# Optimization experiments

Hardware: AMD Instinct MI355X
Metric: run time of the kernel (lower is better)

The kernel has to match this reference:

```python
import jax, jax.numpy as jnp
import numpy as np

WINDOW = 7
SHIFT = 3
NUM_HEADS = 12
DIM = 384
FFN = 4 * DIM
EPS = 1e-5


def _rel_pos_index(w):
    coords = np.stack(np.meshgrid(np.arange(w), np.arange(w), indexing='ij'))  # [2,w,w]
    flat = coords.reshape(2, -1)
    rel = (flat[:, :, None] - flat[:, None, :]).transpose(1, 2, 0)  # [w*w, w*w, 2]
    rel[..., 0] += w - 1
    rel[..., 1] += w - 1
    rel[..., 0] *= 2 * w - 1
    return rel.sum(-1).astype(np.int32)  # [w*w, w*w]


def _attn_mask(hp, wp, w, s):
    # replicate get_attn_mask: region labeling, window partition, pairwise diff
    img = np.zeros((hp, wp), dtype=np.float32)
    cnt = 0
    for hs in (slice(0, -w), slice(-w, -s), slice(-s, None)):
        for ws in (slice(0, -w), slice(-w, -s), slice(-s, None)):
            img[hs, ws] = cnt
            cnt += 1
    mw = img.reshape(hp // w, w, wp // w, w).transpose(0, 2, 1, 3).reshape(-1, w * w)
    diff = mw[:, None, :] - mw[:, :, None]  # unsqueeze(1) - unsqueeze(2)
    return jnp.asarray(np.where(diff != 0, -100.0, 0.0).astype(np.float32))


def _ln(x, g, b):
    mu = jnp.mean(x, -1, keepdims=True)
    var = jnp.mean(jnp.square(x - mu), -1, keepdims=True)
    return (x - mu) * jax.lax.rsqrt(var + EPS) * g + b


def setup_inputs() -> dict:
    key = jax.random.key(0)
    ks = jax.random.split(key, 12)
    B, H, W, C = 8, 56, 56, DIM
    sd = 0.02
    inp = {
        'hidden_states': jax.random.normal(ks[0], (B, H * W, C), jnp.float32),
        'ln1_g': jnp.ones((C,), jnp.float32), 'ln1_b': jnp.zeros((C,), jnp.float32),
        'q_w': jax.random.normal(ks[1], (C, C), jnp.float32) * sd, 'q_b': jnp.zeros((C,), jnp.float32),
        'k_w': jax.random.normal(ks[2], (C, C), jnp.float32) * sd, 'k_b': jnp.zeros((C,), jnp.float32),
        'v_w': jax.random.normal(ks[3], (C, C), jnp.float32) * sd, 'v_b': jnp.zeros((C,), jnp.float32),
        'rpb_table': jax.random.normal(ks[4], ((2 * WINDOW - 1) ** 2, NUM_HEADS), jnp.float32) * sd,
        'rp_index': jnp.asarray(_rel_pos_index(WINDOW)),
        'proj_w': jax.random.normal(ks[5], (C, C), jnp.float32) * sd, 'proj_b': jnp.zeros((C,), jnp.float32),
        'ln2_g': jnp.ones((C,), jnp.float32), 'ln2_b': jnp.zeros((C,), jnp.float32),
        'fc1_w': jax.random.normal(ks[6], (C, FFN), jnp.float32) * sd, 'fc1_b': jnp.zeros((FFN,), jnp.float32),
        'fc2_w': jax.random.normal(ks[7], (FFN, C), jnp.float32) * sd, 'fc2_b': jnp.zeros((C,), jnp.float32),
        'height': H, 'width': W,
    }
    return inp


def reference(hidden_states, ln1_g, ln1_b, q_w, q_b, k_w, k_b, v_w, v_b,
              rpb_table, rp_index, proj_w, proj_b, ln2_g, ln2_b,
              fc1_w, fc1_b, fc2_w, fc2_b, height, width):
    w, s, nh = WINDOW, SHIFT, NUM_HEADS
    B, L, C = hidden_states.shape
    hd = C // nh
    shortcut = hidden_states

    x = _ln(hidden_states, ln1_g, ln1_b).reshape(B, height, width, C)
    pad_b = (w - height % w) % w
    pad_r = (w - width % w) % w
    if pad_b or pad_r:
        x = jnp.pad(x, ((0, 0), (0, pad_b), (0, pad_r), (0, 0)))
    Hp, Wp = height + pad_b, width + pad_r

    if s > 0:
        x = jnp.roll(x, shift=(-s, -s), axis=(1, 2))

    # window partition -> [B*nW, w*w, C]
    N = w * w
    xw = x.reshape(B, Hp // w, w, Wp // w, w, C).transpose(0, 1, 3, 2, 4, 5).reshape(-1, N, C)

    q = (xw @ q_w + q_b).reshape(-1, N, nh, hd).transpose(0, 2, 1, 3)
    k = (xw @ k_w + k_b).reshape(-1, N, nh, hd).transpose(0, 2, 1, 3)
    v = (xw @ v_w + v_b).reshape(-1, N, nh, hd).transpose(0, 2, 1, 3)

    scores = jnp.einsum('whnd,whmd->whnm', q, k) / jnp.sqrt(jnp.float32(hd))
    bias = rpb_table[rp_index.reshape(-1)].reshape(N, N, nh).transpose(2, 0, 1)
    scores = scores + bias[None]

    if s > 0:
        mask = _attn_mask(Hp, Wp, w, s)  # [nW, N, N]
        nW = mask.shape[0]
        scores = scores.reshape(B, nW, nh, N, N) + mask[None, :, None]
        scores = scores.reshape(-1, nh, N, N)

    probs = jax.nn.softmax(scores, axis=-1)
    ctx = jnp.einsum('whnm,whmd->whnd', probs, v).transpose(0, 2, 1, 3).reshape(-1, N, C)
    attn_out = ctx @ proj_w + proj_b

    # window reverse
    xr = attn_out.reshape(B, Hp // w, Wp // w, w, w, C).transpose(0, 1, 3, 2, 4, 5).reshape(B, Hp, Wp, C)
    if s > 0:
        xr = jnp.roll(xr, shift=(s, s), axis=(1, 2))
    if pad_b or pad_r:
        xr = xr[:, :height, :width, :]
    xr = xr.reshape(B, height * width, C)

    h = shortcut + xr
    y = _ln(h, ln2_g, ln2_b)
    y = jax.nn.gelu(y @ fc1_w + fc1_b, approximate=False)
    return h + (y @ fc2_w + fc2_b)
```

## Files before the change

### kernel.cpp

```cpp
#include <hip/hip_runtime.h>
#include <hip/hip_bf16.h>

typedef unsigned short u16;
typedef short bf16x8 __attribute__((ext_vector_type(8)));
typedef float f32x4 __attribute__((ext_vector_type(4)));

__device__ __forceinline__ u16 f2bf(float x) {
  __hip_bfloat16 h = __float2bfloat16(x);
  return *reinterpret_cast<u16*>(&h);
}
__device__ __forceinline__ float bf2f(u16 x) {
  __hip_bfloat16 h = *reinterpret_cast<__hip_bfloat16*>(&x);
  return __bfloat162float(h);
}
__device__ __forceinline__ float rdany(const void* p, size_t i, int f) {
  return f ? ((const float*)p)[i] : bf2f(((const u16*)p)[i]);
}

__device__ __forceinline__ void gld_lds16(const u16* g, u16* l) {
  __builtin_amdgcn_global_load_lds(
      (const __attribute__((address_space(1))) void*)g,
      (__attribute__((address_space(3))) void*)l, 16, 0, 0);
}

__device__ __forceinline__ float gelu_fast(float x) {
  float x2 = x * x;
  float u2 = 1.5957691216057308f * x * __builtin_fmaf(0.044715f, x2, 1.f);
  float e = __expf(u2);
  float r = 1.f / (e + 1.f);
  return x - x * r;
}

__global__ void detect_k(const u16* __restrict__ ln1g_raw, int* __restrict__ flag) {
  if (threadIdx.x == 0 && blockIdx.x == 0)
    *flag = (ln1g_raw[0] == 0 && ln1g_raw[2] == 0) ? 1 : 0;
}

__global__ __launch_bounds__(256) void prep_k(
    const void* qw, const void* kw, const void* vw, const void* pw,
    const void* f1w, const void* f2w,
    u16* __restrict__ qwT, u16* __restrict__ kwT, u16* __restrict__ vwT,
    u16* __restrict__ pwT, u16* __restrict__ f1T, u16* __restrict__ f2T,
    const void* s0, const void* s1, const void* s2, const void* s3,
    const void* s4, const void* s5, const void* s6, const void* s7,
    const void* s8, const void* s9, const void* s10,
    u16* __restrict__ vecdst, const int* __restrict__ rpi,
    u16* __restrict__ biasT, const int* __restrict__ flag) {
  int f = *flag;
  int b = blockIdx.x;
  if (b >= 1728) {
    int tid = threadIdx.y * 32 + threadIdx.x;
    if (b == 1729) {
      for (int i = tid; i < 28812; i += 256) {
        int hh = i / 2401, r = i - hh * 2401;
        biasT[i] = f2bf(rdany(s10, (size_t)rpi[r] * 12 + hh, f));
      }
      return;
    }
    const void* srcs[11] = {s0, s1, s2, s3, s4, s5, s6, s7, s8, s9, s10};
    const int offs[12] = {0, 384, 768, 1152, 1536, 1920, 2304, 2688, 3072, 3456, 4992, 7020};
    for (int i = tid; i < 7020; i += 256) {
      int seg = 0;
#pragma unroll
      for (int t = 1; t < 11; t++) seg += (i >= offs[t]) ? 1 : 0;
      vecdst[i] = f2bf(rdany(srcs[seg], i - offs[seg], f));
    }
    return;
  }
  const void* src; u16* dst; int R, C, bx, by;
  if (b < 576) {
    int m = b / 144, t = b - m * 144;
    src = (m == 0) ? qw : (m == 1) ? kw : (m == 2) ? vw : pw;
    dst = (m == 0) ? qwT : (m == 1) ? kwT : (m == 2) ? vwT : pwT;
    R = 384; C = 384; bx = t % 12; by = t / 12;
  } else if (b < 1152) {
    int t = b - 576; src = f1w; dst = f1T; R = 384; C = 1536;
    bx = t % 48; by = t / 48;
  } else {
    int t = b - 1152; src = f2w; dst = f2T; R = 1536; C = 384;
    bx = t % 12; by = t / 12;
  }
  __shared__ u16 tbuf[32][33];
  int x = threadIdx.x, y = threadIdx.y;
  int gx = bx * 32, gy = by * 32;
#pragma unroll
  for (int j = 0; j < 32; j += 8)
    tbuf[y + j][x] = f2bf(rdany(src, (size_t)(gy + y + j) * C + gx + x, f));
  __syncthreads();
#pragma unroll
  for (int j = 0; j < 32; j += 8) dst[(size_t)(gx + y + j) * R + gy + x] = tbuf[x][y + j];
}

__global__ __launch_bounds__(256) void ln1_window_k(
    const void* __restrict__ hid, const u16* __restrict__ g,
    const u16* __restrict__ b, u16* __restrict__ xw, int rowoff,
    const int* __restrict__ flag) {
  int f = *flag;
  int wv = threadIdx.x >> 6, lane = threadIdx.x & 63;
  int lrow = blockIdx.x * 4 + wv;
  int row = rowoff + lrow;
  int wid = row / 49, n = row - wid * 49;
  int bimg = wid >> 6, w8 = wid & 63;
  int wi = w8 >> 3, wj = w8 & 7;
  int p = n / 7, q = n - p * 7;
  int si = wi * 7 + p + 3; if (si >= 56) si -= 56;
  int sj = wj * 7 + q + 3; if (sj >= 56) sj -= 56;
  size_t src = ((size_t)bimg * 3136 + si * 56 + sj) * 384;
  float x[6]; float s = 0.f, s2 = 0.f;
#pragma unroll
  for (int e = 0; e < 6; e++) {
    x[e] = rdany(hid, src + e * 64 + lane, f);
    s += x[e]; s2 += x[e] * x[e];
  }
#pragma unroll
  for (int off = 32; off; off >>= 1) { s += __shfl_xor(s, off); s2 += __shfl_xor(s2, off); }
  float mu = s * (1.f / 384.f);
  float var = s2 * (1.f / 384.f) - mu * mu;
  float rs = 1.f / sqrtf(var + 1e-5f);
  size_t dst = (size_t)lrow * 384;
#pragma unroll
  for (int e = 0; e < 6; e++) {
    int c = e * 64 + lane;
    float yv = (x[e] - mu) * rs * bf2f(g[c]) + bf2f(b[c]);
    xw[dst + c] = f2bf(yv);
  }
}

__global__ __launch_bounds__(256) void ln2_k(
    const float* hsrc, const u16* __restrict__ g,
    const u16* __restrict__ b, u16* __restrict__ out) {
  int wv = threadIdx.x >> 6, lane = threadIdx.x & 63;
  int row = blockIdx.x * 4 + wv;
  size_t src = (size_t)row * 384;
  float x[6]; float s = 0.f, s2 = 0.f;
#pragma unroll
  for (int e = 0; e < 6; e++) {
    x[e] = hsrc[src + e * 64 + lane];
    s += x[e]; s2 += x[e] * x[e];
  }
#pragma unroll
  for (int off = 32; off; off >>= 1) { s += __shfl_xor(s, off); s2 += __shfl_xor(s2, off); }
  float mu = s * (1.f / 384.f);
  float var = s2 * (1.f / 384.f) - mu * mu;
  float rs = 1.f / sqrtf(var + 1e-5f);
#pragma unroll
  for (int e = 0; e < 6; e++) {
    int c = e * 64 + lane;
    float yv = (x[e] - mu) * rs * bf2f(g[c]) + bf2f(b[c]);
    out[src + c] = f2bf(yv);
  }
}

template <int EPI>
__global__ __launch_bounds__(256, 4) void gemm_bt(
    const u16* __restrict__ A, const u16* __restrict__ Bt,
    const u16* __restrict__ bias, void* outB,
    const void* __restrict__ shortcut, const float* hres,
    int M, int N, int K, int gmoff, int gx, const int* __restrict__ flag) {
  __shared__ __align__(16) u16 As[2][128 * 32];
  __shared__ __align__(16) u16 Bs[2][128 * 32];
  int bx = blockIdx.x;
  if (bx >= gx) return;
  int tid = threadIdx.x;
  int m0 = bx * 128, n0 = blockIdx.y * 128;
  int lane = tid & 63, wv = tid >> 6;
  int wm = (wv >> 1) * 64, wn = (wv & 1) * 64;
  int l15 = lane & 15, quad = lane >> 4;
  f32x4 acc[4][4];
#pragma unroll
  for (int a = 0; a < 4; a++)
#pragma unroll
    for (int c = 0; c < 4; c++) acc[a][c] = (f32x4){0.f, 0.f, 0.f, 0.f};

  int rowS[2], cS[2], wbS[2];
#pragma unroll
  for (int i = 0; i < 2; i++) {
    int id = i * 256 + tid;
    rowS[i] = id >> 2;
    cS[i] = id & 3;
    wbS[i] = (id & ~63) * 8;
  }
  const u16* pA[2]; const u16* pB[2];
#pragma unroll
  for (int i = 0; i < 2; i++) {
    pA[i] = A + (size_t)(m0 + rowS[i]) * K + cS[i] * 8;
    pB[i] = Bt + (size_t)(n0 + rowS[i]) * K + cS[i] * 8;
  }

#pragma unroll
  for (int i = 0; i < 2; i++) {
    gld_lds16(pA[i], &As[0][wbS[i]]);
    gld_lds16(pB[i], &Bs[0][wbS[i]]);
  }
#pragma unroll
  for (int i = 0; i < 2; i++) { pA[i] += 32; pB[i] += 32; }

  int cur = 0;
  for (int kb = 0; kb < K; kb += 32) {
    if (kb + 32 < K) {
#pragma unroll
      for (int i = 0; i < 2; i++) {
        gld_lds16(pA[i], &As[cur ^ 1][wbS[i]]);
        gld_lds16(pB[i], &Bs[cur ^ 1][wbS[i]]);
      }
#pragma unroll
      for (int i = 0; i < 2; i++) { pA[i] += 32; pB[i] += 32; }
      asm volatile("s_waitcnt vmcnt(4)" ::: "memory");
    } else {
      asm volatile("s_waitcnt vmcnt(0)" ::: "memory");
    }
    __builtin_amdgcn_s_barrier();
    __builtin_amdgcn_sched_barrier(0);
    __builtin_amdgcn_s_setprio(1);
    {
      bf16x8 af[4], bfv[4];
#pragma unroll
      for (int mi = 0; mi < 4; mi++)
        af[mi] = *(const bf16x8*)&As[cur][(wm + mi * 16 + l15) * 32 + quad * 8];
#pragma unroll
      for (int ni = 0; ni < 4; ni++)
        bfv[ni] = *(const bf16x8*)&Bs[cur][(wn + ni * 16 + l15) * 32 + quad * 8];
#pragma unroll
      for (int mi = 0; mi < 4; mi++)
#pragma unroll
        for (int ni = 0; ni < 4; ni++)
          acc[mi][ni] = __builtin_amdgcn_mfma_f32_16x16x32_bf16(af[mi], bfv[ni], acc[mi][ni], 0, 0, 0);
    }
    __builtin_amdgcn_s_setprio(0);
    __builtin_amdgcn_sched_barrier(0);
    __builtin_amdgcn_s_barrier();
    cur ^= 1;
  }

  int f = (EPI == 2) ? *flag : 0;
  float biasv[4];
#pragma unroll
  for (int ni = 0; ni < 4; ni++) biasv[ni] = bf2f(bias[n0 + wn + ni * 16 + l15]);
  int seg = n0 / 384;
#pragma unroll
  for (int mi = 0; mi < 4; mi++) {
#pragma unroll
    for (int r = 0; r < 4; r++) {
      int gm = m0 + wm + mi * 16 + quad * 4 + r;
      size_t orow = 0;
      if (EPI == 2) {
        int grow = gmoff + gm;
        int wid = grow / 49, nIn = grow - wid * 49;
        int bimg = wid >> 6, w8 = wid & 63;
        int wi = w8 >> 3, wj = w8 & 7;
        int p = nIn / 7, q = nIn - p * 7;
        int oi = wi * 7 + p + 3; if (oi >= 56) oi -= 56;
        int oj = wj * 7 + q + 3; if (oj >= 56) oj -= 56;
        orow = ((size_t)bimg * 3136 + oi * 56 + oj) * 384;
      }
#pragma unroll
      for (int ni = 0; ni < 4; ni++) {
        int gn = n0 + wn + ni * 16 + l15;
        float v = acc[mi][ni][r] + biasv[ni];
        if (EPI == 1) {
          v = gelu_fast(v);
          ((u16*)outB)[(size_t)gm * N + gn] = f2bf(v);
        } else if (EPI == 2) {
          float hv = rdany(shortcut, orow + gn, f) + v;
          hv = fminf(fmaxf(hv, -1000.f), 1000.f);
          ((float*)outB)[orow + gn] = hv;
        } else if (EPI == 3) {
          float t = v + hres[(size_t)gm * N + gn];
          t = fminf(fmaxf(t, -1000.f), 1000.f);
          ((float*)outB)[(size_t)gm * N + gn] = t;
        } else {
          u16* dst = (u16*)outB + (size_t)seg * M * 384;
          dst[(size_t)gm * 384 + (gn - seg * 384)] = f2bf(v);
        }
      }
    }
  }
}

__global__ __launch_bounds__(256, 5) void attn_k(
    const u16* __restrict__ Q, const u16* __restrict__ Kb, const u16* __restrict__ V,
    const u16* __restrict__ biasT, u16* __restrict__ ctx, int wdoff) {
  __shared__ __align__(16) u16 qs[64 * 56];
  __shared__ __align__(16) u16 ks_[64 * 56];
  __shared__ __align__(16) u16 vt[32 * 72];
  __shared__ __align__(16) u16 P[64 * 72];
  __shared__ int regid[49];
  int lwd = blockIdx.x, hh = blockIdx.y;
  int wd = wdoff + lwd;
  int tid = threadIdx.x;
  int w8 = wd & 63, wi = w8 >> 3, wj = w8 & 7;

  for (int idx = tid; idx < 840; idx += 256) {
    int rr = idx / 56, cc = idx - rr * 56;
    qs[(49 + rr) * 56 + cc] = 0;
    ks_[(49 + rr) * 56 + cc] = 0;
  }
  for (int idx = tid; idx < 480; idx += 256) {
    int d = idx / 15, m = 49 + (idx - d * 15);
    vt[d * 72 + m] = 0;
  }
  if (tid < 49) {
    int p = tid / 7, q = tid - p * 7;
    int rr = (wi == 7) ? (p < 4 ? 1 : 2) : 0;
    int cc = (wj == 7) ? (q < 4 ? 1 : 2) : 0;
    regid[tid] = rr * 3 + cc;
  }
  size_t base = ((size_t)lwd * 49) * 384 + hh * 32;
  for (int idx = tid; idx < 392; idx += 256) {
    int mat = idx >= 196;
    int rid = idx - mat * 196;
    int n = rid >> 2, c = rid & 3;
    uint4 val = *(const uint4*)((mat ? Kb : Q) + base + (size_t)n * 384 + c * 8);
    *(uint4*)&((mat ? ks_ : qs)[n * 56 + c * 8]) = val;
  }
  for (int idx = tid; idx < 196; idx += 256) {
    int n = idx >> 2, c = idx & 3;
    uint4 val = *(const uint4*)(V + base + (size_t)n * 384 + c * 8);
    u16 tmp[8];
    *(uint4*)tmp = val;
#pragma unroll
    for (int t = 0; t < 8; t++) vt[(c * 8 + t) * 72 + n] = tmp[t];
  }
  __syncthreads();

  int lane = tid & 63, wv = tid >> 6, l15 = lane & 15, quad = lane >> 4;
  f32x4 zero = (f32x4){0.f, 0.f, 0.f, 0.f};
  bf16x8 aq = *(const bf16x8*)&qs[(wv * 16 + l15) * 56 + quad * 8];
  f32x4 sc[4];
#pragma unroll
  for (int mi = 0; mi < 4; mi++) {
    bf16x8 bk = *(const bf16x8*)&ks_[(mi * 16 + l15) * 56 + quad * 8];
    sc[mi] = __builtin_amdgcn_mfma_f32_16x16x32_bf16(aq, bk, zero, 0, 0, 0);
  }
  const float scale = 0.17677669529663687f;

  int rm[4];
#pragma unroll
  for (int mi = 0; mi < 4; mi++) {
    int m = mi * 16 + l15;
    rm[mi] = (m < 49) ? regid[m] : -2;
  }
  float pv[4][4];
#pragma unroll
  for (int r = 0; r < 4; r++) {
    int n = wv * 16 + quad * 4 + r;
    int rn = (n < 49) ? regid[n] : -1;
    const u16* brow = biasT + hh * 2401 + n * 49;
#pragma unroll
    for (int mi = 0; mi < 4; mi++) {
      int m = mi * 16 + l15;
      float v = sc[mi][r] * scale;
      if (n < 49 && m < 49) {
        v += bf2f(brow[m]);
        if (rn != rm[mi]) v -= 100.f;
      }
      if (m >= 49) v = -1e4f;
      pv[r][mi] = v;
    }
    float mx = fmaxf(fmaxf(pv[r][0], pv[r][1]), fmaxf(pv[r][2], pv[r][3]));
#pragma unroll
    for (int off = 1; off < 16; off <<= 1) mx = fmaxf(mx, __shfl_xor(mx, off));
    float sum = 0.f;
#pragma unroll
    for (int mi = 0; mi < 4; mi++) {
      pv[r][mi] = __expf(pv[r][mi] - mx);
      sum += pv[r][mi];
    }
#pragma unroll
    for (int off = 1; off < 16; off <<= 1) sum += __shfl_xor(sum, off);
    float inv = 1.f / sum;
#pragma unroll
    for (int mi = 0; mi < 4; mi++)
      P[n * 72 + mi * 16 + l15] = f2bf(pv[r][mi] * inv);
  }

  f32x4 oacc[2]; oacc[0] = zero; oacc[1] = zero;
#pragma unroll
  for (int ks = 0; ks < 2; ks++) {
    bf16x8 ap = *(const bf16x8*)&P[(wv * 16 + l15) * 72 + ks * 32 + quad * 8];
#pragma unroll
    for (int ni = 0; ni < 2; ni++) {
      bf16x8 bv = *(const bf16x8*)&vt[(ni * 16 + l15) * 72 + ks * 32 + quad * 8];
      oacc[ni] = __builtin_amdgcn_mfma_f32_16x16x32_bf16(ap, bv, oacc[ni], 0, 0, 0);
    }
  }
#pragma unroll
  for (int ni = 0; ni < 2; ni++) {
#pragma unroll
    for (int r = 0; r < 4; r++) {
      int n = wv * 16 + quad * 4 + r;
      if (n < 49) {
        int d = ni * 16 + l15;
        ctx[base + (size_t)n * 384 + d] = f2bf(oacc[ni][r]);
      }
    }
  }
}

static inline int pad8(int gx) { return (gx + 7) & ~7; }

extern "C" void kernel_launch(void* const* d_in, const int* in_sizes, int n_in,
                              void* d_out, int out_size, void* d_ws, size_t ws_size,
                              hipStream_t stream) {
  const void* hid = d_in[0];
  const void* ln1g = d_in[1];
  const void* ln1b = d_in[2];
  const void* qw = d_in[3];
  const void* qb = d_in[4];
  const void* kw = d_in[5];
  const void* kbias = d_in[6];
  const void* vw = d_in[7];
  const void* vb = d_in[8];
  const void* rpb = d_in[9];
  const int* rpi = (const int*)d_in[10];
  const void* pw = d_in[11];
  const void* pb = d_in[12];
  const void* ln2g = d_in[13];
  const void* ln2b = d_in[14];
  const void* f1w = d_in[15];
  const void* f1b = d_in[16];
  const void* f2w = d_in[17];
  const void* f2b = d_in[18];

  char* ws = (char*)d_ws;
  u16* wT = (u16*)ws;
  u16* qwT = wT;
  u16* kwT = qwT + 147456;
  u16* vwT = kwT + 147456;
  u16* pwT = vwT + 147456;
  u16* f1T = pwT + 147456;
  u16* f2T = f1T + 589824;
  u16* VEC = (u16*)(ws + 3538944);
  u16* s_ln1g = VEC + 0;
  u16* s_ln1b = VEC + 384;
  u16* s_qkvb = VEC + 768;
  u16* s_pb = VEC + 1920;
  u16* s_ln2g = VEC + 2304;
  u16* s_ln2b = VEC + 2688;
  u16* s_f2b = VEC + 3072;
  u16* s_f1b = VEC + 3456;
  u16* s_rpb = VEC + 4992;
  int* flag = (int*)(ws + 3552984);
  u16* biasT = (u16*)(ws + 3552992);
  const size_t head = 3610624;

  size_t avail = (ws_size > head) ? ws_size - head : 0;
  int rows1 = (avail >= (size_t)25088 * 3072) ? 25088
            : (avail >= (size_t)12544 * 3072) ? 12544 : 6272;
  int rows2 = (avail >= (size_t)25088 * 3840) ? 25088
            : (avail >= (size_t)12544 * 3840) ? 12544 : 3584;

  u16* P1 = (u16*)(ws + head);
  u16* xw = P1;
  u16* Qb = P1 + (size_t)rows1 * 384;
  u16* Kb = Qb + (size_t)rows1 * 384;
  u16* Vb = Kb + (size_t)rows1 * 384;
  u16* y2 = P1;
  u16* f1o = P1 + (size_t)rows2 * 384;
  float* hbuf = (float*)d_out;

  detect_k<<<1, 64, 0, stream>>>((const u16*)ln1g, flag);
  dim3 tb(32, 8);
  prep_k<<<1730, tb, 0, stream>>>(qw, kw, vw, pw, f1w, f2w,
                                  qwT, kwT, vwT, pwT, f1T, f2T,
                                  ln1g, ln1b, qb, kbias, vb, pb, ln2g, ln2b,
                                  f2b, f1b, rpb, VEC, rpi, biasT, flag);

  for (int off = 0; off < 25088; off += rows1) {
    int gx = rows1 / 128;
    ln1_window_k<<<rows1 / 4, 256, 0, stream>>>(hid, s_ln1g, s_ln1b, xw, off, flag);
    gemm_bt<4><<<dim3(pad8(gx), 9), 256, 0, stream>>>(
        xw, qwT, s_qkvb, Qb, nullptr, nullptr, rows1, 1152, 384, 0, gx, flag);
    attn_k<<<dim3(rows1 / 49, 12), 256, 0, stream>>>(Qb, Kb, Vb, biasT, xw, off / 49);
    gemm_bt<2><<<dim3(pad8(gx), 3), 256, 0, stream>>>(
        xw, pwT, s_pb, hbuf, hid, nullptr, rows1, 384, 384, off, gx, flag);
  }

  for (int off = 0; off < 25088; off += rows2) {
    int gx = rows2 / 128;
    ln2_k<<<rows2 / 4, 256, 0, stream>>>(hbuf + (size_t)off * 384, s_ln2g, s_ln2b, y2);
    gemm_bt<1><<<dim3(pad8(gx), 12), 256, 0, stream>>>(
        y2, f1T, s_f1b, f1o, nullptr, nullptr, rows2, 1536, 384, 0, gx, flag);
    gemm_bt<3><<<dim3(pad8(gx), 3), 256, 0, stream>>>(
        f1o, f2T, s_f2b, hbuf + (size_t)off * 384, nullptr,
        hbuf + (size_t)off * 384, rows2, 384, 1536, 0, gx, flag);
  }
}
```

Measured before the change: 397.1 us.

## Replace direct global-to-LDS loads with register-staged loads into padded LDS tiles

The GEMM mainloop no longer uses global_load_lds to write tiles straight into shared memory. Each thread now loads 16 bytes into registers, computes on the current buffer, then writes the prefetched data into a padded LDS layout (row stride 36 instead of 32) to reduce bank conflicts on fragment reads. Fragment reads are split into two 8-byte LDS loads because the padding breaks 16-byte alignment. The change trades away the async direct-to-LDS path, adding register pressure, extra LDS instructions and an additional barrier per K step.

```diff
diff --git a/kernel.cpp b/kernel.cpp
--- a/kernel.cpp
+++ b/kernel.cpp
@@ -15,12 +15,6 @@
 }
 __device__ __forceinline__ float rdany(const void* p, size_t i, int f) {
   return f ? ((const float*)p)[i] : bf2f(((const u16*)p)[i]);
-}
-
-__device__ __forceinline__ void gld_lds16(const u16* g, u16* l) {
-  __builtin_amdgcn_global_load_lds(
-      (const __attribute__((address_space(1))) void*)g,
-      (__attribute__((address_space(3))) void*)l, 16, 0, 0);
 }
 
 __device__ __forceinline__ float gelu_fast(float x) {
@@ -157,8 +151,8 @@
     const u16* __restrict__ bias, void* outB,
     const void* __restrict__ shortcut, const float* hres,
     int M, int N, int K, int gmoff, int gx, const int* __restrict__ flag) {
-  __shared__ __align__(16) u16 As[2][128 * 32];
-  __shared__ __align__(16) u16 Bs[2][128 * 32];
+  __shared__ __align__(16) u16 As[2][128 * 36];
+  __shared__ __align__(16) u16 Bs[2][128 * 36];
   int bx = blockIdx.x;
   if (bx >= gx) return;
   int tid = threadIdx.x;
@@ -172,13 +166,13 @@
 #pragma unroll
     for (int c = 0; c < 4; c++) acc[a][c] = (f32x4){0.f, 0.f, 0.f, 0.f};
 
-  int rowS[2], cS[2], wbS[2];
+  int rowS[2], cS[2], ldsW[2];
 #pragma unroll
   for (int i = 0; i < 2; i++) {
     int id = i * 256 + tid;
     rowS[i] = id >> 2;
     cS[i] = id & 3;
-    wbS[i] = (id & ~63) * 8;
+    ldsW[i] = rowS[i] * 36 + cS[i] * 8;
   }
   const u16* pA[2]; const u16* pB[2];
 #pragma unroll
@@ -187,39 +181,49 @@
     pB[i] = Bt + (size_t)(n0 + rowS[i]) * K + cS[i] * 8;
   }
 
+  uint4 ra[2], rb[2];
+#pragma unroll
+  for (int i = 0; i < 2; i++) { ra[i] = *(const uint4*)pA[i]; rb[i] = *(const uint4*)pB[i]; }
+#pragma unroll
+  for (int i = 0; i < 2; i++) { pA[i] += 32; pB[i] += 32; }
 #pragma unroll
   for (int i = 0; i < 2; i++) {
-    gld_lds16(pA[i], &As[0][wbS[i]]);
-    gld_lds16(pB[i], &Bs[0][wbS[i]]);
-  }
-#pragma unroll
-  for (int i = 0; i < 2; i++) { pA[i] += 32; pB[i] += 32; }
+    *(uint2*)&As[0][ldsW[i]] = make_uint2(ra[i].x, ra[i].y);
+    *(uint2*)&As[0][ldsW[i] + 4] = make_uint2(ra[i].z, ra[i].w);
+    *(uint2*)&Bs[0][ldsW[i]] = make_uint2(rb[i].x, rb[i].y);
+    *(uint2*)&Bs[0][ldsW[i] + 4] = make_uint2(rb[i].z, rb[i].w);
+  }
+  __syncthreads();
 
   int cur = 0;
   for (int kb = 0; kb < K; kb += 32) {
-    if (kb + 32 < K) {
-#pragma unroll
-      for (int i = 0; i < 2; i++) {
-        gld_lds16(pA[i], &As[cur ^ 1][wbS[i]]);
-        gld_lds16(pB[i], &Bs[cur ^ 1][wbS[i]]);
-      }
+    bool more = (kb + 32 < K);
+    if (more) {
+#pragma unroll
+      for (int i = 0; i < 2; i++) { ra[i] = *(const uint4*)pA[i]; rb[i] = *(const uint4*)pB[i]; }
 #pragma unroll
       for (int i = 0; i < 2; i++) { pA[i] += 32; pB[i] += 32; }
-      asm volatile("s_waitcnt vmcnt(4)" ::: "memory");
-    } else {
-      asm volatile("s_waitcnt vmcnt(0)" ::: "memory");
-    }
-    __builtin_amdgcn_s_barrier();
+    }
     __builtin_amdgcn_sched_barrier(0);
     __builtin_amdgcn_s_setprio(1);
     {
       bf16x8 af[4], bfv[4];
 #pragma unroll
-      for (int mi = 0; mi < 4; mi++)
-        af[mi] = *(const bf16x8*)&As[cur][(wm + mi * 16 + l15) * 32 + quad * 8];
-#pragma unroll
-      for (int ni = 0; ni < 4; ni++)
-        bfv[ni] = *(const bf16x8*)&Bs[cur][(wn + ni * 16 + l15) * 32 + quad * 8];
+      for (int mi = 0; mi < 4; mi++) {
+        int base = (wm + mi * 16 + l15) * 36 + quad * 8;
+        union { uint2 h[2]; bf16x8 v; } u;
+        u.h[0] = *(const uint2*)&As[cur][base];
+        u.h[1] = *(const uint2*)&As[cur][base + 4];
+        af[mi] = u.v;
+      }
+#pragma unroll
+      for (int ni = 0; ni < 4; ni++) {
+        int base = (wn + ni * 16 + l15) * 36 + quad * 8;
+        union { uint2 h[2]; bf16x8 v; } u;
+        u.h[0] = *(const uint2*)&Bs[cur][base];
+        u.h[1] = *(const uint2*)&Bs[cur][base + 4];
+        bfv[ni] = u.v;
+      }
 #pragma unroll
       for (int mi = 0; mi < 4; mi++)
 #pragma unroll
@@ -228,7 +232,17 @@
     }
     __builtin_amdgcn_s_setprio(0);
     __builtin_amdgcn_sched_barrier(0);
-    __builtin_amdgcn_s_barrier();
+    __syncthreads();
+    if (more) {
+#pragma unroll
+      for (int i = 0; i < 2; i++) {
+        *(uint2*)&As[cur ^ 1][ldsW[i]] = make_uint2(ra[i].x, ra[i].y);
+        *(uint2*)&As[cur ^ 1][ldsW[i] + 4] = make_uint2(ra[i].z, ra[i].w);
+        *(uint2*)&Bs[cur ^ 1][ldsW[i]] = make_uint2(rb[i].x, rb[i].y);
+        *(uint2*)&Bs[cur ^ 1][ldsW[i] + 4] = make_uint2(rb[i].z, rb[i].w);
+      }
+    }
+    __syncthreads();
     cur ^= 1;
   }
 
```

Result: no change. 392.1 us (-1.2%).
